# Kernel optimization log

Measured on AMD Instinct MI355X. Metric: run time of the kernel, lower is better.

The kernel has to match this reference:

```python
import jax, jax.numpy as jnp
import numpy as np

B, L, D, V, C = 128, 128, 512, 50000, 512  # batch, leaves, embed_dim, vocab, num_category
NODES = 2 * L - 1


def setup_inputs() -> dict:
    key = jax.random.key(0)
    k1, k2, k3, k4 = jax.random.split(key, 4)
    leaf_content_id = jax.random.randint(k1, (B, L), 0, V)
    # leaves occupy positions 0..L-1; internal nodes fill L..2L-2 during compose
    content_mask = jnp.concatenate(
        [jnp.ones((B, L), dtype=bool), jnp.zeros((B, L - 1), dtype=bool)], axis=1)
    # each step composes two already-available nodes; leaf indices are always valid
    composition_info = jax.random.randint(k2, (B, L - 1, 2), 0, L)
    emb_weight = jax.random.normal(k3, (V, D), dtype=jnp.float32) * 0.02
    lin_w = jax.random.normal(k4, (C, D), dtype=jnp.float32) * 0.02
    lin_b = jnp.zeros((C,), dtype=jnp.float32)
    return dict(leaf_content_id=leaf_content_id, content_mask=content_mask,
                composition_info=composition_info, emb_weight=emb_weight,
                lin_w=lin_w, lin_b=lin_b)


def circular_correlation(a, b):
    # corr(a, b) = irfft(conj(rfft(a)) * rfft(b))
    fa = jnp.fft.rfft(a, axis=-1)
    fb = jnp.fft.rfft(b, axis=-1)
    return jnp.fft.irfft(jnp.conj(fa) * fb, n=a.shape[-1], axis=-1)


def reference(leaf_content_id, content_mask, composition_info, emb_weight, lin_w, lin_b):
    Bq, Lq = leaf_content_id.shape
    nodes = 2 * Lq - 1
    Dq = emb_weight.shape[1]
    # embed leaves into positions where content_mask is True (first L slots)
    leaf_vec = emb_weight[leaf_content_id]                      # [B, L, D]
    vector = jnp.zeros((Bq, nodes, Dq), dtype=emb_weight.dtype)
    vector = vector.at[:, :Lq].set(jnp.where(content_mask[:, :Lq, None], leaf_vec, 0.0))
    batch_ar = jnp.arange(Bq)

    def step(vec, xs):
        idx, li, ri = xs                                        # li, ri: [B]
        left = vec[batch_ar, li]                                # gather [B, D]
        right = vec[batch_ar, ri]
        comp = circular_correlation(left, right)                # [B, D]
        # internal node for step idx lands at position L + idx (rolled mask)
        vec = jax.lax.dynamic_update_slice(vec, comp[:, None, :], (0, Lq + idx, 0))
        return vec, None

    xs = (jnp.arange(Lq - 1),
          composition_info[:, :, 0].T.astype(jnp.int32),
          composition_info[:, :, 1].T.astype(jnp.int32))
    vector, _ = jax.lax.scan(step, vector, xs)
    logits = jnp.einsum('bnd,cd->bnc', vector, lin_w) + lin_b   # [B, 2L-1, C]
    return jax.nn.sigmoid(logits)
```

## Files before the change

### kernel.cpp

```cpp
#include <hip/hip_runtime.h>
#include <hip/hip_bf16.h>

#define Bq 128
#define Lq 128
#define Dq 512
#define NODES 255
#define Cq 512
#define M_ROWS (Bq * NODES)
#define FP8_SCALE 64.0f
#define INV_SCALE2 (1.0f / (FP8_SCALE * FP8_SCALE))

typedef unsigned int uint32;
typedef unsigned char uchar;
typedef _Float16 v8hf __attribute__((ext_vector_type(8)));
typedef __fp16 v2fp __attribute__((ext_vector_type(2)));
typedef float v4f __attribute__((ext_vector_type(4)));
typedef unsigned int v4u __attribute__((ext_vector_type(4)));

__device__ inline uint32 packh(float lo, float hi) {
    v2fp p = __builtin_amdgcn_cvt_pkrtz(lo, hi);
    return __builtin_bit_cast(uint32, p);
}
__device__ inline uint32 fp8x4(float a, float b, float c, float d) {
    int lo = __builtin_amdgcn_cvt_pk_fp8_f32(a, b, 0, false);
    return (uint32)__builtin_amdgcn_cvt_pk_fp8_f32(c, d, lo, true);
}
__device__ inline uchar fp8b(float a) {
    return (uchar)(__builtin_amdgcn_cvt_pk_fp8_f32(a, a, 0, false) & 0xFF);
}

__global__ __launch_bounds__(256) void wconv_kernel(const float* __restrict__ linw,
                                                    uchar* __restrict__ wb) {
    int i = (blockIdx.x * 256 + threadIdx.x) * 8;
    float4 v0 = *((const float4*)(linw + i));
    float4 v1 = *((const float4*)(linw + i + 4));
    uint2 o;
    o.x = fp8x4(v0.x * FP8_SCALE, v0.y * FP8_SCALE, v0.z * FP8_SCALE, v0.w * FP8_SCALE);
    o.y = fp8x4(v1.x * FP8_SCALE, v1.y * FP8_SCALE, v1.z * FP8_SCALE, v1.w * FP8_SCALE);
    *((uint2*)(wb + i)) = o;
}

#define CW2 1296

__global__ __launch_bounds__(512, 4) void fused_kernel(const int* __restrict__ ids,
                                                       const int* __restrict__ cinfo,
                                                       const float* __restrict__ emb,
                                                       const uchar* __restrict__ wb,
                                                       const float* __restrict__ bias,
                                                       float* __restrict__ out) {
    __shared__ __align__(16) uchar smem[32768 + CW2 * 4 * 8];
    uchar* Vt = smem;
    uint32* scratch = (uint32*)(smem + 32768);
    int t = threadIdx.x;
    int wave = t >> 6, lane = t & 63;
    int blk = blockIdx.x;

    uint32* W = scratch + wave * CW2;
    int q = lane >> 4, m = lane & 15;
#pragma unroll
    for (int ri = 0; ri < 8; ++ri) {
        int r = ri * 8 + wave;
        int R = blk * 64 + r;
        int b = R / 255;
        int node = R - b * 255;
        int key = (r & 7) << 4;
        uchar* vrow = Vt + r * 512;
        if (node < Lq) {
            int id = ids[b * Lq + node];
            const float* src = emb + (size_t)id * Dq + lane * 8;
            float4 v0 = *((const float4*)src);
            float4 v1 = *((const float4*)(src + 4));
            uint2 o;
            o.x = fp8x4(v0.x * FP8_SCALE, v0.y * FP8_SCALE, v0.z * FP8_SCALE, v0.w * FP8_SCALE);
            o.y = fp8x4(v1.x * FP8_SCALE, v1.y * FP8_SCALE, v1.z * FP8_SCALE, v1.w * FP8_SCALE);
            int byte = (((lane >> 1) << 4) ^ key) | ((lane & 1) << 3);
            *((uint2*)(vrow + byte)) = o;
        } else {
            int idx = node - Lq;
            int li = cinfo[(b * (Lq - 1) + idx) * 2 + 0];
            int rx = cinfo[(b * (Lq - 1) + idx) * 2 + 1];
            int lid = ids[b * Lq + li];
            int rid = ids[b * Lq + rx];
            const float4* lr = (const float4*)(emb + (size_t)lid * Dq);
            const float4* rr = (const float4*)(emb + (size_t)rid * Dq);
            float4 a0 = lr[2 * lane], a1 = lr[2 * lane + 1];
            float4 c0 = rr[2 * lane], c1 = rr[2 * lane + 1];
            v4u ua = {packh(a0.x, a0.y), packh(a0.z, a0.w), packh(a1.x, a1.y), packh(a1.z, a1.w)};
            v4u ub = {packh(c0.x, c0.y), packh(c0.z, c0.w), packh(c1.x, c1.y), packh(c1.z, c1.w)};
            ((v4u*)(W))[lane] = ua;
            ((v4u*)(W + 256))[lane] = ua;
            ((v4u*)(W + 512))[lane] = ub;
            ((v4u*)(W + 768))[lane] = ub;
            uint32 dn = (uint32)__shfl((int)ub.x, (lane + 1) & 63);
            v4u uo;
            uo.x = __builtin_amdgcn_alignbit(ub.y, ub.x, 16);
            uo.y = __builtin_amdgcn_alignbit(ub.z, ub.y, 16);
            uo.z = __builtin_amdgcn_alignbit(ub.w, ub.z, 16);
            uo.w = __builtin_amdgcn_alignbit(dn,   ub.w, 16);
            ((v4u*)(W + 1028))[lane] = uo;
            if (lane < 2) ((v4u*)(W + 1284))[lane] = uo;

            const uint32* A0 = W + (4 * q - 8 * m + 256);
            const uint32* A1 = W + (4 * q - 8 * m + 128);
            const uint32* PB = W + ((lane & 1) ? 1028 : 512) + 4 * q + (m >> 1);
            v4f acc0 = {0.f, 0.f, 0.f, 0.f};
            v4f acc1 = {0.f, 0.f, 0.f, 0.f};
#pragma unroll
            for (int kb = 0; kb < 16; ++kb) {
                v4u Ra = *((const v4u*)(A0 + 16 * kb));
                v4u Rb = *((const v4u*)(A1 + 16 * kb));
                v4u RB;
                RB.x = PB[16 * kb + 0]; RB.y = PB[16 * kb + 1];
                RB.z = PB[16 * kb + 2]; RB.w = PB[16 * kb + 3];
                v8hf fa0 = __builtin_bit_cast(v8hf, Ra);
                v8hf fa1 = __builtin_bit_cast(v8hf, Rb);
                v8hf fb  = __builtin_bit_cast(v8hf, RB);
                acc0 = __builtin_amdgcn_mfma_f32_16x16x32_f16(fa0, fb, acc0, 0, 0, 0);
                acc1 = __builtin_amdgcn_mfma_f32_16x16x32_f16(fa1, fb, acc1, 0, 0, 0);
            }
#pragma unroll
            for (int rr2 = 0; rr2 < 4; ++rr2) {
                int ch = 4 * q + rr2;
                vrow[(((ch)      << 4) ^ key) | m] = fp8b(acc0[rr2] * FP8_SCALE);
                vrow[(((ch + 16) << 4) ^ key) | m] = fp8b(acc1[rr2] * FP8_SCALE);
            }
        }
    }

    int quad = lane >> 4, qq = lane & 15;
    int qhi = quad >> 1, qlo = quad & 1;
    int cw = wave * 64;

    const uchar* wp[4];
#pragma unroll
    for (int i = 0; i < 4; ++i)
        wp[i] = wb + (size_t)(cw + 16 * i + qq) * Dq + 8 * quad;
    long wreg[4];
#pragma unroll
    for (int i = 0; i < 4; ++i)
        wreg[i] = *((const long*)(wp[i]));

    __syncthreads();

    v4f acc[4][4];
#pragma unroll
    for (int i = 0; i < 4; ++i)
#pragma unroll
        for (int j = 0; j < 4; ++j)
            acc[i][j] = (v4f){0.f, 0.f, 0.f, 0.f};

#pragma unroll
    for (int ks = 0; ks < 16; ++ks) {
        long wcur[4];
#pragma unroll
        for (int i = 0; i < 4; ++i) wcur[i] = wreg[i];
        if (ks < 15) {
#pragma unroll
            for (int i = 0; i < 4; ++i)
                wreg[i] = *((const long*)(wp[i] + 32 * (ks + 1)));
        }
        long vf[4];
#pragma unroll
        for (int j = 0; j < 4; ++j) {
            int row = 16 * j + qq;
            int phys = (2 * ks + qhi) ^ (qq & 7);
            vf[j] = *((const long*)(Vt + row * 512 + phys * 16 + qlo * 8));
        }
#pragma unroll
        for (int i = 0; i < 4; ++i)
#pragma unroll
            for (int j = 0; j < 4; ++j)
                acc[i][j] = __builtin_amdgcn_mfma_f32_16x16x32_fp8_fp8(wcur[i], vf[j], acc[i][j], 0, 0, 0);
    }

#pragma unroll
    for (int i = 0; i < 4; ++i) {
        int cb = cw + 16 * i + 4 * quad;
        float4 b4 = *((const float4*)(bias + cb));
#pragma unroll
        for (int j = 0; j < 4; ++j) {
            int grow = blk * 64 + 16 * j + qq;
            float4 o4;
            o4.x = 1.f / (1.f + __expf(-(acc[i][j][0] * INV_SCALE2 + b4.x)));
            o4.y = 1.f / (1.f + __expf(-(acc[i][j][1] * INV_SCALE2 + b4.y)));
            o4.z = 1.f / (1.f + __expf(-(acc[i][j][2] * INV_SCALE2 + b4.z)));
            o4.w = 1.f / (1.f + __expf(-(acc[i][j][3] * INV_SCALE2 + b4.w)));
            *((float4*)(out + (size_t)grow * Cq + cb)) = o4;
        }
    }
}

extern "C" void kernel_launch(void* const* d_in, const int* in_sizes, int n_in,
                              void* d_out, int out_size, void* d_ws, size_t ws_size,
                              hipStream_t stream) {
    const int*   ids   = (const int*)d_in[0];
    const int*   cinfo = (const int*)d_in[2];
    const float* emb   = (const float*)d_in[3];
    const float* linw  = (const float*)d_in[4];
    const float* linb  = (const float*)d_in[5];
    float* out = (float*)d_out;

    uchar* wb = (uchar*)d_ws;

    wconv_kernel<<<dim3(128), dim3(256), 0, stream>>>(linw, wb);
    fused_kernel<<<dim3(M_ROWS / 64), dim3(512), 0, stream>>>(ids, cinfo, emb, wb, linb, out);

    (void)in_sizes; (void)n_in; (void)out_size; (void)ws_size;
}
```

Measured before the change: 214.5 us.

## Prefetch embedding rows one iteration ahead and shrink per-wave scratch

Loads all node ids and composition indices up front, then software-pipelines the embedding-row fetches so row ri+1's global loads are in flight while row ri is converted or composed. Leaf rows fetch the same row twice so the loop body stays uniform. The per-wave LDS scratch shrinks by dropping most of the duplicate B copy, and s_setprio is raised around the main FP8 MFMA block. This costs extra registers and redundant loads for leaf rows, and it depends on the circular wraparound reads staying inside the smaller scratch layout.

```diff
diff --git a/kernel.cpp b/kernel.cpp
--- a/kernel.cpp
+++ b/kernel.cpp
@@ -40,7 +40,7 @@
     *((uint2*)(wb + i)) = o;
 }
 
-#define CW2 1296
+#define CW2 1040
 
 __global__ __launch_bounds__(512, 4) void fused_kernel(const int* __restrict__ ids,
                                                        const int* __restrict__ cinfo,
@@ -57,52 +57,68 @@
 
     uint32* W = scratch + wave * CW2;
     int q = lane >> 4, m = lane & 15;
+
+    int aid[8], cid[8];
+#pragma unroll
+    for (int ri = 0; ri < 8; ++ri) {
+        int R = blk * 64 + ri * 8 + wave;
+        int b = R / 255;
+        int node = R - b * 255;
+        int leaf = node < Lq;
+        int idx = leaf ? 0 : node - Lq;
+        int li = cinfo[(b * (Lq - 1) + idx) * 2 + 0];
+        int rx = cinfo[(b * (Lq - 1) + idx) * 2 + 1];
+        aid[ri] = ids[b * Lq + (leaf ? node : li)];
+        cid[ri] = leaf ? -1 : ids[b * Lq + rx];
+    }
+
+    float4 pa0, pa1, pc0, pc1;
+    {
+        const float4* ar = (const float4*)(emb + (size_t)aid[0] * Dq);
+        int cn = cid[0] < 0 ? aid[0] : cid[0];
+        const float4* cr = (const float4*)(emb + (size_t)cn * Dq);
+        pa0 = ar[2 * lane]; pa1 = ar[2 * lane + 1];
+        pc0 = cr[2 * lane]; pc1 = cr[2 * lane + 1];
+    }
 #pragma unroll
     for (int ri = 0; ri < 8; ++ri) {
         int r = ri * 8 + wave;
-        int R = blk * 64 + r;
-        int b = R / 255;
-        int node = R - b * 255;
+        float4 a0 = pa0, a1 = pa1, c0 = pc0, c1 = pc1;
+        bool leaf = cid[ri] < 0;
+        if (ri < 7) {
+            const float4* ar = (const float4*)(emb + (size_t)aid[ri + 1] * Dq);
+            int cn = cid[ri + 1] < 0 ? aid[ri + 1] : cid[ri + 1];
+            const float4* cr = (const float4*)(emb + (size_t)cn * Dq);
+            pa0 = ar[2 * lane]; pa1 = ar[2 * lane + 1];
+            pc0 = cr[2 * lane]; pc1 = cr[2 * lane + 1];
+        }
         int key = (r & 7) << 4;
         uchar* vrow = Vt + r * 512;
-        if (node < Lq) {
-            int id = ids[b * Lq + node];
-            const float* src = emb + (size_t)id * Dq + lane * 8;
-            float4 v0 = *((const float4*)src);
-            float4 v1 = *((const float4*)(src + 4));
+        if (leaf) {
             uint2 o;
-            o.x = fp8x4(v0.x * FP8_SCALE, v0.y * FP8_SCALE, v0.z * FP8_SCALE, v0.w * FP8_SCALE);
-            o.y = fp8x4(v1.x * FP8_SCALE, v1.y * FP8_SCALE, v1.z * FP8_SCALE, v1.w * FP8_SCALE);
+            o.x = fp8x4(a0.x * FP8_SCALE, a0.y * FP8_SCALE, a0.z * FP8_SCALE, a0.w * FP8_SCALE);
+            o.y = fp8x4(a1.x * FP8_SCALE, a1.y * FP8_SCALE, a1.z * FP8_SCALE, a1.w * FP8_SCALE);
             int byte = (((lane >> 1) << 4) ^ key) | ((lane & 1) << 3);
             *((uint2*)(vrow + byte)) = o;
         } else {
-            int idx = node - Lq;
-            int li = cinfo[(b * (Lq - 1) + idx) * 2 + 0];
-            int rx = cinfo[(b * (Lq - 1) + idx) * 2 + 1];
-            int lid = ids[b * Lq + li];
-            int rid = ids[b * Lq + rx];
-            const float4* lr = (const float4*)(emb + (size_t)lid * Dq);
-            const float4* rr = (const float4*)(emb + (size_t)rid * Dq);
-            float4 a0 = lr[2 * lane], a1 = lr[2 * lane + 1];
-            float4 c0 = rr[2 * lane], c1 = rr[2 * lane + 1];
             v4u ua = {packh(a0.x, a0.y), packh(a0.z, a0.w), packh(a1.x, a1.y), packh(a1.z, a1.w)};
             v4u ub = {packh(c0.x, c0.y), packh(c0.z, c0.w), packh(c1.x, c1.y), packh(c1.z, c1.w)};
             ((v4u*)(W))[lane] = ua;
             ((v4u*)(W + 256))[lane] = ua;
             ((v4u*)(W + 512))[lane] = ub;
-            ((v4u*)(W + 768))[lane] = ub;
+            if (lane < 2) ((v4u*)(W + 768))[lane] = ub;
             uint32 dn = (uint32)__shfl((int)ub.x, (lane + 1) & 63);
             v4u uo;
             uo.x = __builtin_amdgcn_alignbit(ub.y, ub.x, 16);
             uo.y = __builtin_amdgcn_alignbit(ub.z, ub.y, 16);
             uo.z = __builtin_amdgcn_alignbit(ub.w, ub.z, 16);
             uo.w = __builtin_amdgcn_alignbit(dn,   ub.w, 16);
-            ((v4u*)(W + 1028))[lane] = uo;
-            if (lane < 2) ((v4u*)(W + 1284))[lane] = uo;
+            ((v4u*)(W + 776))[lane] = uo;
+            if (lane < 2) ((v4u*)(W + 1032))[lane] = uo;
 
             const uint32* A0 = W + (4 * q - 8 * m + 256);
             const uint32* A1 = W + (4 * q - 8 * m + 128);
-            const uint32* PB = W + ((lane & 1) ? 1028 : 512) + 4 * q + (m >> 1);
+            const uint32* PB = W + ((lane & 1) ? 776 : 512) + 4 * q + (m >> 1);
             v4f acc0 = {0.f, 0.f, 0.f, 0.f};
             v4f acc1 = {0.f, 0.f, 0.f, 0.f};
 #pragma unroll
@@ -166,11 +182,13 @@
             int phys = (2 * ks + qhi) ^ (qq & 7);
             vf[j] = *((const long*)(Vt + row * 512 + phys * 16 + qlo * 8));
         }
+        __builtin_amdgcn_s_setprio(1);
 #pragma unroll
         for (int i = 0; i < 4; ++i)
 #pragma unroll
             for (int j = 0; j < 4; ++j)
                 acc[i][j] = __builtin_amdgcn_mfma_f32_16x16x32_fp8_fp8(wcur[i], vf[j], acc[i][j], 0, 0, 0);
+        __builtin_amdgcn_s_setprio(0);
     }
 
 #pragma unroll
```

After: 213.3 us. About the same (-0.6%).
